# Optimization experiments

Measured on AMD Instinct MI355X. Metric: run time of the kernel, lower is better.

Reference implementation:

```python
import jax, jax.numpy as jnp
import numpy as np

MAX_TRAV = 21  # matches the torch module constant


def setup_inputs() -> dict:
    key = jax.random.key(0)
    k1, _ = jax.random.split(key)
    B, H, W = 4, 2048, 2048
    untraversable = jax.random.randint(k1, (B, H, W), 0, 2).astype(jnp.bool_)
    max_sq = jnp.ones((1,), dtype=jnp.float32) * float(MAX_TRAV ** 2)  # 441.0
    return {"untraversable": untraversable, "max_sq": max_sq}


def _chamfer(untraversable, max_sq):
    big = max_sq[0]
    B, H, W = untraversable.shape
    # 0 at obstacles, MAX_TRAV^2 elsewhere (values are small exact ints in fp32)
    sq = jnp.where(untraversable, jnp.float32(0.0), big)
    # odd increments 1,3,...,41: cumulative sum of first k odds = k^2
    ds = jnp.arange(1, 2 * MAX_TRAV + 1, 2, dtype=jnp.float32)

    col = jnp.full((B, H, 1), big, dtype=jnp.float32)

    def hstep(s, d):
        from_right = jnp.concatenate([s[:, :, 1:] + d, col], axis=2)
        from_left = jnp.concatenate([col, s[:, :, :-1] + d], axis=2)
        return jnp.minimum(s, jnp.minimum(from_right, from_left)), None

    sq, _ = jax.lax.scan(hstep, sq, ds)

    row = jnp.full((B, 1, W), big, dtype=jnp.float32)

    def vstep(s, d):
        from_below = jnp.concatenate([s[:, 1:, :] + d, row], axis=1)
        from_above = jnp.concatenate([row, s[:, :-1, :] + d], axis=1)
        return jnp.minimum(s, jnp.minimum(from_below, from_above)), None

    sq, _ = jax.lax.scan(vstep, sq, ds)
    return jnp.sqrt(sq)


def reference(untraversable, max_sq):
    return _chamfer(untraversable, max_sq)
```

## Files before the change

### kernel.cpp

```cpp
#include <hip/hip_runtime.h>
#include <cstdint>

#define BB 4
#define HH 2048
#define WW 2048
#define MAXT 21
#define BIGSQ 441

static __device__ __forceinline__ uint32_t umin32(uint32_t a, uint32_t b) { return a < b ? a : b; }

__global__ __launch_bounds__(256, 4) void hpass(const int* __restrict__ in,
                                                uint8_t* __restrict__ dh) {
    const int tid  = threadIdx.x;
    const int lane = tid & 63;
    const int w    = tid >> 6;
    const int row  = (blockIdx.x << 2) + w;
    const long long ro = (long long)row * WW;
    const int* rp = in + ro;
    const int li = 63 - lane;

    uint2 u[16];
    #pragma unroll
    for (int c = 0; c < 16; ++c)
        u[c] = *(const uint2*)(rp + (c << 7) + (lane << 1));

    unsigned long long b0p = 0, b1p = 0;
    unsigned long long b0c = __ballot(u[0].x != 0);
    unsigned long long b1c = __ballot(u[0].y != 0);

    #pragma unroll
    for (int c = 0; c < 16; ++c) {
        unsigned long long b0n = 0, b1n = 0;
        if (c < 15) {
            b0n = __ballot(u[c + 1].x != 0);
            b1n = __ballot(u[c + 1].y != 0);
        }
        unsigned long long rb0c = __brevll(b1c), rb1c = __brevll(b0c);
        unsigned long long rb0p = __brevll(b1p), rb1p = __brevll(b0p);

        unsigned long long S0  = (b0c >> lane) | ((b0n << 1) << li);
        unsigned long long S1  = (b1c >> lane) | ((b1n << 1) << li);
        unsigned long long SL0 = (rb0c >> li)  | ((rb0p << 1) << lane);
        unsigned long long SL1 = (rb1c >> li)  | ((rb1p << 1) << lane);

        const uint32_t SEN = 1u << 11;
        uint32_t s0 = (uint32_t)S0, s1 = (uint32_t)S1;
        uint32_t l0 = (uint32_t)SL0, l1 = (uint32_t)SL1;
        int t_s0  = __builtin_ctz(s0 | SEN);
        int t_s1  = __builtin_ctz(s1 | SEN);
        int t_s0s = __builtin_ctz((s0 >> 1) | SEN);
        int t_l0  = __builtin_ctz(l0 | SEN);
        int t_l1  = __builtin_ctz(l1 | SEN);
        int t_l0s = __builtin_ctz((l0 >> 1) | SEN);

        int d0 = min(min(2 * t_s0, 2 * t_s1 + 1), min(2 * t_l1, 2 * t_l0s + 1));
        int d1 = min(min(2 * t_s1, 2 * t_s0s + 1), min(2 * t_l0, 2 * t_l1 + 1));
        d0 = min(d0, MAXT);
        d1 = min(d1, MAXT);

        *(uint16_t*)(dh + ro + (c << 7) + (lane << 1)) = (uint16_t)(d0 | (d1 << 8));

        b0p = b0c; b1p = b1c; b0c = b0n; b1c = b1n;
    }
}

__global__ __launch_bounds__(256) void vpass(const uint8_t* __restrict__ dh,
                                             float* __restrict__ out) {
    __shared__ uint16_t s[106][128];
    const int tid = threadIdx.x;
    const int x0  = blockIdx.x << 7;
    const int y0  = blockIdx.y << 6;
    const int b   = blockIdx.z;
    const long long base = (long long)b * HH * WW;

    for (int i = tid; i < 106 * 16; i += 256) {
        int r  = i >> 4;
        int c8 = (i & 15) << 3;
        int gy = y0 - 21 + r;
        uint4 pk;
        if (gy >= 0 && gy < HH) {
            const uint8_t* p = dh + base + (long long)gy * WW + x0 + c8;
            uint2 uu = *(const uint2*)p;
            uint32_t e0 = uu.x & 0xff, e1 = (uu.x >> 8) & 0xff, e2 = (uu.x >> 16) & 0xff, e3 = uu.x >> 24;
            uint32_t e4 = uu.y & 0xff, e5 = (uu.y >> 8) & 0xff, e6 = (uu.y >> 16) & 0xff, e7 = uu.y >> 24;
            pk.x = (e0 * e0) | ((e1 * e1) << 16);
            pk.y = (e2 * e2) | ((e3 * e3) << 16);
            pk.z = (e4 * e4) | ((e5 * e5) << 16);
            pk.w = (e6 * e6) | ((e7 * e7) << 16);
        } else {
            pk.x = pk.y = pk.z = pk.w = BIGSQ | (BIGSQ << 16);
        }
        *(uint4*)&s[r][c8] = pk;
    }
    __syncthreads();

    const int lane = tid & 63;
    const int w    = tid >> 6;
    const int cg   = (lane & 31) << 2;
    const int ro   = lane >> 5;
    for (int k = 0; k < 8; ++k) {
        const int j  = (w << 4) + (k << 1) + ro;
        const int yl = 21 + j;

        uint2 q = *(const uint2*)&s[yl][cg];
        uint32_t v0 = q.x & 0xffff, v1 = q.x >> 16;
        uint32_t v2 = q.y & 0xffff, v3 = q.y >> 16;

        for (int d = 1; d <= MAXT; ++d) {
            const uint32_t dd = (uint32_t)(d * d);
            uint32_t h  = v0 > v1 ? v0 : v1;
            uint32_t h2 = v2 > v3 ? v2 : v3;
            h = h > h2 ? h : h2;
            if (__all(dd >= h)) break;
            uint2 a  = *(const uint2*)&s[yl - d][cg];
            uint2 bq = *(const uint2*)&s[yl + d][cg];
            const uint32_t dd2 = dd * 0x10001u;
            uint32_t A0 = a.x + dd2, A1 = a.y + dd2;
            uint32_t B0 = bq.x + dd2, B1 = bq.y + dd2;
            v0 = umin32(v0, umin32(A0 & 0xffff, B0 & 0xffff));
            v1 = umin32(v1, umin32(A0 >> 16,    B0 >> 16));
            v2 = umin32(v2, umin32(A1 & 0xffff, B1 & 0xffff));
            v3 = umin32(v3, umin32(A1 >> 16,    B1 >> 16));
        }

        float4 o;
        o.x = sqrtf((float)v0);
        o.y = sqrtf((float)v1);
        o.z = sqrtf((float)v2);
        o.w = sqrtf((float)v3);
        *(float4*)&out[base + (long long)(y0 + j) * WW + x0 + cg] = o;
    }
}

extern "C" void kernel_launch(void* const* d_in, const int* in_sizes, int n_in,
                              void* d_out, int out_size, void* d_ws, size_t ws_size,
                              hipStream_t stream) {
    const int* unt = (const int*)d_in[0];
    uint8_t* dh    = (uint8_t*)d_ws;
    float* out     = (float*)d_out;

    hpass<<<dim3(BB * HH / 4), 256, 0, stream>>>(unt, dh);
    vpass<<<dim3(WW / 128, HH / 64, BB), 256, 0, stream>>>(dh, out);
}
```

Before: 40.97 us.

## Fuse horizontal and vertical passes into one tiled kernel with halo recompute

Merges the horizontal distance pass into the vertical pass kernel. Each block recomputes horizontal distances for its 106-row tile, using ballots plus 64-column left and right halos, and writes squared values straight into shared memory. This drops the intermediate workspace write and read and one kernel launch. In exchange, the input rows in the vertical halo (42 of 106) are read and processed redundantly, so input traffic grows by roughly 1.66x, and the per-row work is less well amortised.

```diff
diff --git a/kernel.cpp b/kernel.cpp
--- a/kernel.cpp
+++ b/kernel.cpp
@@ -6,98 +6,77 @@
 #define WW 2048
 #define MAXT 21
 #define BIGSQ 441
+#define TROWS 106
 
 static __device__ __forceinline__ uint32_t umin32(uint32_t a, uint32_t b) { return a < b ? a : b; }
 
-__global__ __launch_bounds__(256, 4) void hpass(const int* __restrict__ in,
-                                                uint8_t* __restrict__ dh) {
+__global__ __launch_bounds__(256) void fused(const int* __restrict__ in,
+                                             float* __restrict__ out) {
+    __shared__ uint16_t s[TROWS][128];
     const int tid  = threadIdx.x;
     const int lane = tid & 63;
     const int w    = tid >> 6;
-    const int row  = (blockIdx.x << 2) + w;
-    const long long ro = (long long)row * WW;
-    const int* rp = in + ro;
-    const int li = 63 - lane;
+    const int x0   = blockIdx.x << 7;
+    const int y0   = blockIdx.y << 6;
+    const int b    = blockIdx.z;
+    const long long base = (long long)b * HH * WW;
+    const int li   = 63 - lane;
+    const int hl2  = (lane & 31) << 1;
+    const bool hasL = (x0 > 0);
+    const bool hasR = (x0 + 128 < WW);
 
-    uint2 u[16];
-    #pragma unroll
-    for (int c = 0; c < 16; ++c)
-        u[c] = *(const uint2*)(rp + (c << 7) + (lane << 1));
+    for (int r = w; r < TROWS; r += 4) {
+        const int gy = y0 - 21 + r;
+        uint32_t pk;
+        if (gy >= 0 && gy < HH) {
+            const int* rp = in + base + (long long)gy * WW;
+            uint2 uc = *(const uint2*)(rp + x0 + (lane << 1));
+            unsigned long long b0c = __ballot(uc.x != 0);
+            unsigned long long b1c = __ballot(uc.y != 0);
+            unsigned long long b0p = 0, b1p = 0, b0n = 0, b1n = 0;
+            if (hasL) {
+                uint2 hl = *(const uint2*)(rp + x0 - 64 + hl2);
+                b0p = __ballot(lane < 32 && hl.x != 0) << 32;
+                b1p = __ballot(lane < 32 && hl.y != 0) << 32;
+            }
+            if (hasR) {
+                uint2 hr = *(const uint2*)(rp + x0 + 128 + hl2);
+                b0n = __ballot(lane < 32 && hr.x != 0);
+                b1n = __ballot(lane < 32 && hr.y != 0);
+            }
 
-    unsigned long long b0p = 0, b1p = 0;
-    unsigned long long b0c = __ballot(u[0].x != 0);
-    unsigned long long b1c = __ballot(u[0].y != 0);
+            unsigned long long rb0c = __brevll(b1c), rb1c = __brevll(b0c);
+            unsigned long long rb0p = __brevll(b1p), rb1p = __brevll(b0p);
 
-    #pragma unroll
-    for (int c = 0; c < 16; ++c) {
-        unsigned long long b0n = 0, b1n = 0;
-        if (c < 15) {
-            b0n = __ballot(u[c + 1].x != 0);
-            b1n = __ballot(u[c + 1].y != 0);
+            unsigned long long S0  = (b0c >> lane) | ((b0n << 1) << li);
+            unsigned long long S1  = (b1c >> lane) | ((b1n << 1) << li);
+            unsigned long long SL0 = (rb0c >> li)  | ((rb0p << 1) << lane);
+            unsigned long long SL1 = (rb1c >> li)  | ((rb1p << 1) << lane);
+
+            const uint32_t SEN = 1u << 11;
+            uint32_t s0 = (uint32_t)S0, s1 = (uint32_t)S1;
+            uint32_t l0 = (uint32_t)SL0, l1 = (uint32_t)SL1;
+            int t_s0  = __builtin_ctz(s0 | SEN);
+            int t_s1  = __builtin_ctz(s1 | SEN);
+            int t_s0s = __builtin_ctz((s0 >> 1) | SEN);
+            int t_l0  = __builtin_ctz(l0 | SEN);
+            int t_l1  = __builtin_ctz(l1 | SEN);
+            int t_l0s = __builtin_ctz((l0 >> 1) | SEN);
+
+            int d0 = min(min(2 * t_s0, 2 * t_s1 + 1), min(2 * t_l1, 2 * t_l0s + 1));
+            int d1 = min(min(2 * t_s1, 2 * t_s0s + 1), min(2 * t_l0, 2 * t_l1 + 1));
+            d0 = min(d0, MAXT);
+            d1 = min(d1, MAXT);
+            pk = (uint32_t)(d0 * d0) | ((uint32_t)(d1 * d1) << 16);
+        } else {
+            pk = BIGSQ | (BIGSQ << 16);
         }
-        unsigned long long rb0c = __brevll(b1c), rb1c = __brevll(b0c);
-        unsigned long long rb0p = __brevll(b1p), rb1p = __brevll(b0p);
-
-        unsigned long long S0  = (b0c >> lane) | ((b0n << 1) << li);
-        unsigned long long S1  = (b1c >> lane) | ((b1n << 1) << li);
-        unsigned long long SL0 = (rb0c >> li)  | ((rb0p << 1) << lane);
-        unsigned long long SL1 = (rb1c >> li)  | ((rb1p << 1) << lane);
-
-        const uint32_t SEN = 1u << 11;
-        uint32_t s0 = (uint32_t)S0, s1 = (uint32_t)S1;
-        uint32_t l0 = (uint32_t)SL0, l1 = (uint32_t)SL1;
-        int t_s0  = __builtin_ctz(s0 | SEN);
-        int t_s1  = __builtin_ctz(s1 | SEN);
-        int t_s0s = __builtin_ctz((s0 >> 1) | SEN);
-        int t_l0  = __builtin_ctz(l0 | SEN);
-        int t_l1  = __builtin_ctz(l1 | SEN);
-        int t_l0s = __builtin_ctz((l0 >> 1) | SEN);
-
-        int d0 = min(min(2 * t_s0, 2 * t_s1 + 1), min(2 * t_l1, 2 * t_l0s + 1));
-        int d1 = min(min(2 * t_s1, 2 * t_s0s + 1), min(2 * t_l0, 2 * t_l1 + 1));
-        d0 = min(d0, MAXT);
-        d1 = min(d1, MAXT);
-
-        *(uint16_t*)(dh + ro + (c << 7) + (lane << 1)) = (uint16_t)(d0 | (d1 << 8));
-
-        b0p = b0c; b1p = b1c; b0c = b0n; b1c = b1n;
-    }
-}
-
-__global__ __launch_bounds__(256) void vpass(const uint8_t* __restrict__ dh,
-                                             float* __restrict__ out) {
-    __shared__ uint16_t s[106][128];
-    const int tid = threadIdx.x;
-    const int x0  = blockIdx.x << 7;
-    const int y0  = blockIdx.y << 6;
-    const int b   = blockIdx.z;
-    const long long base = (long long)b * HH * WW;
-
-    for (int i = tid; i < 106 * 16; i += 256) {
-        int r  = i >> 4;
-        int c8 = (i & 15) << 3;
-        int gy = y0 - 21 + r;
-        uint4 pk;
-        if (gy >= 0 && gy < HH) {
-            const uint8_t* p = dh + base + (long long)gy * WW + x0 + c8;
-            uint2 uu = *(const uint2*)p;
-            uint32_t e0 = uu.x & 0xff, e1 = (uu.x >> 8) & 0xff, e2 = (uu.x >> 16) & 0xff, e3 = uu.x >> 24;
-            uint32_t e4 = uu.y & 0xff, e5 = (uu.y >> 8) & 0xff, e6 = (uu.y >> 16) & 0xff, e7 = uu.y >> 24;
-            pk.x = (e0 * e0) | ((e1 * e1) << 16);
-            pk.y = (e2 * e2) | ((e3 * e3) << 16);
-            pk.z = (e4 * e4) | ((e5 * e5) << 16);
-            pk.w = (e6 * e6) | ((e7 * e7) << 16);
-        } else {
-            pk.x = pk.y = pk.z = pk.w = BIGSQ | (BIGSQ << 16);
-        }
-        *(uint4*)&s[r][c8] = pk;
+        *(uint32_t*)&s[r][lane << 1] = pk;
     }
     __syncthreads();
 
-    const int lane = tid & 63;
-    const int w    = tid >> 6;
-    const int cg   = (lane & 31) << 2;
-    const int ro   = lane >> 5;
+    const int cg = (lane & 31) << 2;
+    const int ro = lane >> 5;
     for (int k = 0; k < 8; ++k) {
         const int j  = (w << 4) + (k << 1) + ro;
         const int yl = 21 + j;
@@ -136,9 +115,6 @@
                               void* d_out, int out_size, void* d_ws, size_t ws_size,
                               hipStream_t stream) {
     const int* unt = (const int*)d_in[0];
-    uint8_t* dh    = (uint8_t*)d_ws;
     float* out     = (float*)d_out;
-
-    hpass<<<dim3(BB * HH / 4), 256, 0, stream>>>(unt, dh);
-    vpass<<<dim3(WW / 128, HH / 64, BB), 256, 0, stream>>>(dh, out);
+    fused<<<dim3(WW / 128, HH / 64, BB), 256, 0, stream>>>(unt, out);
 }
```

Result: slower. 83.91 us (+104.8%).
